# Optimization experiments

Measured on AMD Instinct MI355X. Metric: run time of the kernel, lower is better.

The kernel has to match this reference:

```python
import jax, jax.numpy as jnp
import numpy as np
import math

B, T, D, H, L = 64, 255, 512, 8, 8
CODEBOOK = 512
V = CODEBOOK + 3  # bos/eos/pad
COND_DIM = 512
MAX_LEN = 256
HD = D // H


def _layernorm(x, g, b, eps=1e-5):
    mu = jnp.mean(x, axis=-1, keepdims=True)
    var = jnp.mean(jnp.square(x - mu), axis=-1, keepdims=True)
    return (x - mu) * jax.lax.rsqrt(var + eps) * g + b


def setup_inputs() -> dict:
    key = jax.random.key(0)
    ks = jax.random.split(key, 24)
    s = 0.02
    d = {
        'tokens': jax.random.randint(ks[0], (B, T), 0, V),
        'cond': jax.random.normal(ks[1], (B, COND_DIM), jnp.float32),
        'emb': jax.random.normal(ks[2], (V, D), jnp.float32) * s,  # tied token_emb / head weight
        'pos_emb': jax.random.normal(ks[3], (1, MAX_LEN, D), jnp.float32) * s,
        'cond_w1': jax.random.normal(ks[4], (COND_DIM, D), jnp.float32) * s,
        'cond_b1': jnp.zeros((D,), jnp.float32),
        'cond_w2': jax.random.normal(ks[5], (D, D), jnp.float32) * s,
        'cond_b2': jnp.zeros((D,), jnp.float32),
        'ln1_g': jnp.ones((L, D), jnp.float32),
        'ln1_b': jnp.zeros((L, D), jnp.float32),
        'qkv_w': jax.random.normal(ks[6], (L, D, 3 * D), jnp.float32) * s,
        'qkv_b': jnp.zeros((L, 3 * D), jnp.float32),
        'proj_w': jax.random.normal(ks[7], (L, D, D), jnp.float32) * s,
        'proj_b': jnp.zeros((L, D), jnp.float32),
        'ln2_g': jnp.ones((L, D), jnp.float32),
        'ln2_b': jnp.zeros((L, D), jnp.float32),
        'mlp_w1': jax.random.normal(ks[8], (L, D, 4 * D), jnp.float32) * s,
        'mlp_b1': jnp.zeros((L, 4 * D), jnp.float32),
        'mlp_w2': jax.random.normal(ks[9], (L, 4 * D, D), jnp.float32) * s,
        'mlp_b2': jnp.zeros((L, D), jnp.float32),
        'lnf_g': jnp.ones((D,), jnp.float32),
        'lnf_b': jnp.zeros((D,), jnp.float32),
    }
    return d


def reference(tokens, cond, emb, pos_emb, cond_w1, cond_b1, cond_w2, cond_b2,
              ln1_g, ln1_b, qkv_w, qkv_b, proj_w, proj_b,
              ln2_g, ln2_b, mlp_w1, mlp_b1, mlp_w2, mlp_b2, lnf_g, lnf_b):
    b, t = tokens.shape
    h = emb[tokens] + pos_emb[:, :t, :]                              # [B,T,D]
    c = jax.nn.silu(cond @ cond_w1 + cond_b1) @ cond_w2 + cond_b2    # [B,D]
    h = jnp.concatenate([c[:, None, :], h], axis=1)                  # [B,S,D]
    S = t + 1
    causal = jnp.tril(jnp.ones((S, S), bool))
    scale = 1.0 / math.sqrt(HD)
    for i in range(L):
        x = _layernorm(h, ln1_g[i], ln1_b[i])
        qkv = (x @ qkv_w[i] + qkv_b[i]).reshape(b, S, 3, H, HD).transpose(2, 0, 3, 1, 4)
        q, k, v = qkv[0], qkv[1], qkv[2]                             # [B,H,S,hd]
        a = jnp.einsum('bhsd,bhtd->bhst', q, k) * scale
        a = jnp.where(causal, a, -jnp.inf)
        a = jax.nn.softmax(a, axis=-1)
        o = jnp.einsum('bhst,bhtd->bhsd', a, v).transpose(0, 2, 1, 3).reshape(b, S, D)
        h = h + o @ proj_w[i] + proj_b[i]
        x = _layernorm(h, ln2_g[i], ln2_b[i])
        h = h + jax.nn.gelu(x @ mlp_w1[i] + mlp_b1[i], approximate=False) @ mlp_w2[i] + mlp_b2[i]
    h = _layernorm(h, lnf_g, lnf_b)
    return (h @ emb.T)[:, 1:, :]                                     # [B,T,V]
```

## Files before the change

### kernel.cpp

```cpp
#include <hip/hip_runtime.h>
#include <hip/hip_bf16.h>

typedef __attribute__((ext_vector_type(8))) short bf16x8;
typedef __attribute__((ext_vector_type(4))) float f32x4;
typedef __attribute__((ext_vector_type(4))) unsigned short u16x4;
typedef __attribute__((ext_vector_type(8))) unsigned short u16x8;
typedef unsigned short u16;

#define DEV static __device__ __forceinline__

DEV float bf2f(u16 u) {
  union { unsigned int i; float f; } c; c.i = ((unsigned int)u) << 16; return c.f;
}
DEV u16 f2bf(float f) {
  union { float f; unsigned int i; } c; c.f = f;
  unsigned int i = c.i;
  i += 0x7FFFu + ((i >> 16) & 1u);
  return (u16)(i >> 16);
}

DEV void gload_lds16(const void* g, void* l) {
  __builtin_amdgcn_global_load_lds((const __attribute__((address_space(1))) void*)g,
                                   (__attribute__((address_space(3))) void*)l, 16, 0, 0);
}

DEV f32x4 mfma16(bf16x8 a, bf16x8 b, f32x4 c) {
  return __builtin_amdgcn_mfma_f32_16x16x32_bf16(a, b, c, 0, 0, 0);
}

__global__ __launch_bounds__(256) void ktranspose(const float* __restrict__ in, u16* __restrict__ out,
                                                  int K, int N) {
  __shared__ u16 tile[32][33];
  const float* src = in + (size_t)blockIdx.z * K * N;
  u16* dst = out + (size_t)blockIdx.z * K * N;
  const int n0 = blockIdx.x * 32, k0 = blockIdx.y * 32;
  const int tx = threadIdx.x, ty = threadIdx.y;
#pragma unroll
  for (int i = ty; i < 32; i += 8) tile[i][tx] = f2bf(src[(size_t)(k0 + i) * N + n0 + tx]);
  __syncthreads();
#pragma unroll
  for (int i = ty; i < 32; i += 8) dst[(size_t)(n0 + i) * K + k0 + tx] = tile[tx][i];
}

__global__ __launch_bounds__(256) void kcvt(const float* __restrict__ in, u16* __restrict__ out, int n) {
  int i = blockIdx.x * 256 + threadIdx.x;
  if (i < n) out[i] = f2bf(in[i]);
}

__global__ __launch_bounds__(256) void kcond(const float* __restrict__ cond, const float* __restrict__ w1,
                                             const float* __restrict__ b1, const float* __restrict__ w2,
                                             const float* __restrict__ b2, float* __restrict__ h) {
  __shared__ float xr[512];
  __shared__ float t1[512];
  const int b = blockIdx.x, tid = threadIdx.x;
  for (int i = tid; i < 512; i += 256) xr[i] = cond[b * 512 + i];
  __syncthreads();
  for (int j = tid; j < 512; j += 256) {
    float acc = b1[j];
    for (int k = 0; k < 512; ++k) acc += xr[k] * w1[k * 512 + j];
    t1[j] = acc / (1.f + __expf(-acc));
  }
  __syncthreads();
  for (int j = tid; j < 512; j += 256) {
    float acc = b2[j];
    for (int k = 0; k < 512; ++k) acc += t1[k] * w2[k * 512 + j];
    h[(size_t)b * 256 * 512 + j] = acc;
  }
}

__global__ __launch_bounds__(256) void kembed(const int* __restrict__ tok, const float* __restrict__ emb,
                                              const float* __restrict__ pos, float* __restrict__ h) {
  const int idx = blockIdx.x;
  const int b = idx / 255, t = idx % 255;
  const int c = threadIdx.x * 2;
  const int tk = tok[idx];
  float2 ev = *(const float2*)(emb + (size_t)tk * 512 + c);
  float2 pv = *(const float2*)(pos + (size_t)t * 512 + c);
  float2 r;
  r.x = ev.x + pv.x;
  r.y = ev.y + pv.y;
  *(float2*)(h + ((size_t)b * 256 + 1 + t) * 512 + c) = r;
}

__global__ __launch_bounds__(64) void kln(const float* __restrict__ hin, const float* __restrict__ g,
                                          const float* __restrict__ bt, u16* __restrict__ out) {
  const int row = blockIdx.x, lane = threadIdx.x;
  const float4* x = (const float4*)(hin + (size_t)row * 512);
  float4 v0 = x[lane], v1 = x[lane + 64];
  float s1 = v0.x + v0.y + v0.z + v0.w + v1.x + v1.y + v1.z + v1.w;
  float s2 = v0.x * v0.x + v0.y * v0.y + v0.z * v0.z + v0.w * v0.w +
             v1.x * v1.x + v1.y * v1.y + v1.z * v1.z + v1.w * v1.w;
#pragma unroll
  for (int off = 1; off < 64; off <<= 1) { s1 += __shfl_xor(s1, off); s2 += __shfl_xor(s2, off); }
  float mu = s1 * (1.f / 512.f);
  float var = s2 * (1.f / 512.f) - mu * mu;
  float rs = rsqrtf(var + 1e-5f);
  const int c0 = lane * 4;
  float4 g0 = *(const float4*)(g + c0), g1 = *(const float4*)(g + 256 + c0);
  float4 b0 = *(const float4*)(bt + c0), b1 = *(const float4*)(bt + 256 + c0);
  u16x4 o0, o1;
  o0[0] = f2bf((v0.x - mu) * rs * g0.x + b0.x);
  o0[1] = f2bf((v0.y - mu) * rs * g0.y + b0.y);
  o0[2] = f2bf((v0.z - mu) * rs * g0.z + b0.z);
  o0[3] = f2bf((v0.w - mu) * rs * g0.w + b0.w);
  o1[0] = f2bf((v1.x - mu) * rs * g1.x + b1.x);
  o1[1] = f2bf((v1.y - mu) * rs * g1.y + b1.y);
  o1[2] = f2bf((v1.z - mu) * rs * g1.z + b1.z);
  o1[3] = f2bf((v1.w - mu) * rs * g1.w + b1.w);
  *(u16x4*)(out + (size_t)row * 512 + c0) = o0;
  *(u16x4*)(out + (size_t)row * 512 + 256 + c0) = o1;
}

template<int MODE>
__global__ __launch_bounds__(256, 2) void kgemm(const u16* __restrict__ A, const u16* __restrict__ Bt,
                                                const float* __restrict__ bias, void* __restrict__ Cout,
                                                int M, int N, int K) {
  __shared__ __align__(16) u16 As[2][4096];
  __shared__ __align__(16) u16 Bs[2][4096];
  const int tid = threadIdx.x;
  const int lane = tid & 63;
  const int wr = tid >> 7, wc = (tid >> 6) & 1;
  const int m0 = blockIdx.x * 128, n0 = blockIdx.y * 128;
  const int nkt = K >> 5;
  const int Kb = K * 2;

  const int c0 = tid * 16;
  const int ar0 = c0 >> 6, ao0 = c0 & 63;
  const int ar1 = (c0 + 4096) >> 6, ao1 = (c0 + 4096) & 63;
  int br0 = n0 + ar0, br1 = n0 + ar1;
  if (MODE == 3) { br0 = min(br0, N - 1); br1 = min(br1, N - 1); }
  const char* Ab = (const char*)A;
  const char* Bb = (const char*)Bt;
  const size_t a0 = (size_t)(m0 + ar0) * Kb + ao0;
  const size_t a1 = (size_t)(m0 + ar1) * Kb + ao1;
  const size_t b0 = (size_t)br0 * Kb + ao0;
  const size_t b1 = (size_t)br1 * Kb + ao1;

  f32x4 acc[4][4];
#pragma unroll
  for (int i = 0; i < 4; ++i)
#pragma unroll
    for (int j = 0; j < 4; ++j) acc[i][j] = f32x4{0.f, 0.f, 0.f, 0.f};

  gload_lds16(Ab + a0, (char*)As[0] + c0);
  gload_lds16(Ab + a1, (char*)As[0] + c0 + 4096);
  gload_lds16(Bb + b0, (char*)Bs[0] + c0);
  gload_lds16(Bb + b1, (char*)Bs[0] + c0 + 4096);
  __syncthreads();

  const int aoff = (wr * 64 + (lane & 15)) * 32 + (lane >> 4) * 8;
  const int boff = (wc * 64 + (lane & 15)) * 32 + (lane >> 4) * 8;

  int buf = 0;
  for (int kt = 0; kt < nkt; ++kt) {
    if (kt + 1 < nkt) {
      const size_t ko = (size_t)(kt + 1) * 64;
      gload_lds16(Ab + a0 + ko, (char*)As[buf ^ 1] + c0);
      gload_lds16(Ab + a1 + ko, (char*)As[buf ^ 1] + c0 + 4096);
      gload_lds16(Bb + b0 + ko, (char*)Bs[buf ^ 1] + c0);
      gload_lds16(Bb + b1 + ko, (char*)Bs[buf ^ 1] + c0 + 4096);
    }
    bf16x8 aF[4], bF[4];
#pragma unroll
    for (int mt = 0; mt < 4; ++mt) aF[mt] = *(const bf16x8*)&As[buf][aoff + mt * 512];
#pragma unroll
    for (int nt = 0; nt < 4; ++nt) bF[nt] = *(const bf16x8*)&Bs[buf][boff + nt * 512];
#pragma unroll
    for (int mt = 0; mt < 4; ++mt)
#pragma unroll
      for (int nt = 0; nt < 4; ++nt)
        acc[mt][nt] = mfma16(aF[mt], bF[nt], acc[mt][nt]);
    __syncthreads();
    buf ^= 1;
  }

  float bv[4];
#pragma unroll
  for (int nt = 0; nt < 4; ++nt) {
    int col = n0 + wc * 64 + nt * 16 + (lane & 15);
    bv[nt] = (MODE == 3) ? 0.f : bias[col];
  }

  if (MODE == 0 || MODE == 1) {
    u16* C = (u16*)Cout;
#pragma unroll
    for (int mt = 0; mt < 4; ++mt)
#pragma unroll
      for (int r = 0; r < 4; ++r) {
        int row = m0 + wr * 64 + mt * 16 + (lane >> 4) * 4 + r;
        u16* cp = C + (size_t)row * N + n0 + wc * 64 + (lane & 15);
#pragma unroll
        for (int nt = 0; nt < 4; ++nt) {
          float v = acc[mt][nt][r] + bv[nt];
          if (MODE == 1) v = 0.5f * v * (1.f + erff(v * 0.70710678118f));
          cp[nt * 16] = f2bf(v);
        }
      }
  } else if (MODE == 2) {
    float* hC = (float*)Cout;
#pragma unroll
    for (int mt = 0; mt < 4; ++mt)
#pragma unroll
      for (int r = 0; r < 4; ++r) {
        int row = m0 + wr * 64 + mt * 16 + (lane >> 4) * 4 + r;
        float* hp = hC + (size_t)row * N + n0 + wc * 64 + (lane & 15);
#pragma unroll
        for (int nt = 0; nt < 4; ++nt) hp[nt * 16] += acc[mt][nt][r] + bv[nt];
      }
  } else {
    float* C = (float*)Cout;
#pragma unroll
    for (int mt = 0; mt < 4; ++mt)
#pragma unroll
      for (int r = 0; r < 4; ++r) {
        int row = m0 + wr * 64 + mt * 16 + (lane >> 4) * 4 + r;
        int s = row & 255;
        if (s == 0) continue;
        int bb = row >> 8;
        float* cp = C + ((size_t)bb * 255 + (s - 1)) * 515 + n0 + wc * 64 + (lane & 15);
#pragma unroll
        for (int nt = 0; nt < 4; ++nt) {
          int col = n0 + wc * 64 + nt * 16 + (lane & 15);
          if (col < 515) cp[nt * 16] = acc[mt][nt][r];
        }
      }
  }
}

__global__ __launch_bounds__(256, 1) void kattn(const u16* __restrict__ qkv, u16* __restrict__ o) {
  __shared__ __align__(16) u16 Ks[256][72];
  __shared__ __align__(16) u16 Vt[64][264];
  __shared__ __align__(16) u16 Ps[4][64][72];
  const int tid = threadIdx.x, wv = tid >> 6, lane = tid & 63;
  const int bh = blockIdx.x, bb = bh >> 3, hh = bh & 7;
  const size_t base = (size_t)bb * 256 * 1536 + hh * 64;

  for (int c = tid; c < 2048; c += 256) {
    int s = c >> 3, pp = c & 7;
    u16x8 kv = *(const u16x8*)(qkv + base + (size_t)s * 1536 + 512 + pp * 8);
    *(u16x8*)&Ks[s][pp * 8] = kv;
    u16x8 vv = *(const u16x8*)(qkv + base + (size_t)s * 1536 + 1024 + pp * 8);
#pragma unroll
    for (int j = 0; j < 8; ++j) Vt[pp * 8 + j][s] = vv[j];
  }
  __syncthreads();

  bf16x8 qf[4][2];
#pragma unroll
  for (int mt = 0; mt < 4; ++mt)
#pragma unroll
    for (int ks = 0; ks < 2; ++ks)
      qf[mt][ks] = *(const bf16x8*)(qkv + base +
                   (size_t)(wv * 64 + mt * 16 + (lane & 15)) * 1536 + ks * 32 + (lane >> 4) * 8);

  const float scale = 0.125f;
  float mrow[4][4], lsum[4][4];
#pragma unroll
  for (int mt = 0; mt < 4; ++mt)
#pragma unroll
    for (int r = 0; r < 4; ++r) { mrow[mt][r] = -1e30f; lsum[mt][r] = 0.f; }

  for (int ct = 0; ct <= wv; ++ct) {
    f32x4 sacc[4][4];
#pragma unroll
    for (int i = 0; i < 4; ++i)
#pragma unroll
      for (int j = 0; j < 4; ++j) sacc[i][j] = f32x4{0.f, 0.f, 0.f, 0.f};
#pragma unroll
    for (int ks = 0; ks < 2; ++ks) {
      bf16x8 kf[4];
#pragma unroll
      for (int nt = 0; nt < 4; ++nt)
        kf[nt] = *(const bf16x8*)&Ks[ct * 64 + nt * 16 + (lane & 15)][ks * 32 + (lane >> 4) * 8];
#pragma unroll
      for (int mt = 0; mt < 4; ++mt)
#pragma unroll
        for (int nt = 0; nt < 4; ++nt)
          sacc[mt][nt] = mfma16(qf[mt][ks], kf[nt], sacc[mt][nt]);
    }
#pragma unroll
    for (int mt = 0; mt < 4; ++mt)
#pragma unroll
      for (int r = 0; r < 4; ++r) {
        int srow = wv * 64 + mt * 16 + (lane >> 4) * 4 + r;
        float mx = -1e30f;
#pragma unroll
        for (int nt = 0; nt < 4; ++nt) {
          int tcol = ct * 64 + nt * 16 + (lane & 15);
          float v = sacc[mt][nt][r] * scale;
          if (tcol > srow) v = -1e30f;
          mx = fmaxf(mx, v);
        }
#pragma unroll
        for (int off = 1; off < 16; off <<= 1) mx = fmaxf(mx, __shfl_xor(mx, off));
        mrow[mt][r] = fmaxf(mrow[mt][r], mx);
      }
  }

  f32x4 oacc[4][4];
#pragma unroll
  for (int i = 0; i < 4; ++i)
#pragma unroll
    for (int j = 0; j < 4; ++j) oacc[i][j] = f32x4{0.f, 0.f, 0.f, 0.f};

  for (int ct = 0; ct <= wv; ++ct) {
    f32x4 sacc[4][4];
#pragma unroll
    for (int i = 0; i < 4; ++i)
#pragma unroll
      for (int j = 0; j < 4; ++j) sacc[i][j] = f32x4{0.f, 0.f, 0.f, 0.f};
#pragma unroll
    for (int ks = 0; ks < 2; ++ks) {
      bf16x8 kf[4];
#pragma unroll
      for (int nt = 0; nt < 4; ++nt)
        kf[nt] = *(const bf16x8*)&Ks[ct * 64 + nt * 16 + (lane & 15)][ks * 32 + (lane >> 4) * 8];
#pragma unroll
      for (int mt = 0; mt < 4; ++mt)
#pragma unroll
        for (int nt = 0; nt < 4; ++nt)
          sacc[mt][nt] = mfma16(qf[mt][ks], kf[nt], sacc[mt][nt]);
    }
#pragma unroll
    for (int mt = 0; mt < 4; ++mt)
#pragma unroll
      for (int r = 0; r < 4; ++r) {
        int srow = wv * 64 + mt * 16 + (lane >> 4) * 4 + r;
        float ps = 0.f;
#pragma unroll
        for (int nt = 0; nt < 4; ++nt) {
          int tcol = ct * 64 + nt * 16 + (lane & 15);
          float v = sacc[mt][nt][r] * scale;
          float pe = (tcol > srow) ? 0.f : __expf(v - mrow[mt][r]);
          ps += pe;
          Ps[wv][mt * 16 + (lane >> 4) * 4 + r][nt * 16 + (lane & 15)] = f2bf(pe);
        }
#pragma unroll
        for (int off = 1; off < 16; off <<= 1) ps += __shfl_xor(ps, off);
        lsum[mt][r] += ps;
      }
#pragma unroll
    for (int ks = 0; ks < 2; ++ks) {
      bf16x8 pf[4], vf[4];
#pragma unroll
      for (int mt = 0; mt < 4; ++mt)
        pf[mt] = *(const bf16x8*)&Ps[wv][mt * 16 + (lane & 15)][ks * 32 + (lane >> 4) * 8];
#pragma unroll
      for (int nt = 0; nt < 4; ++nt)
        vf[nt] = *(const bf16x8*)&Vt[nt * 16 + (lane & 15)][ct * 64 + ks * 32 + (lane >> 4) * 8];
#pragma unroll
      for (int mt = 0; mt < 4; ++mt)
#pragma unroll
        for (int nt = 0; nt < 4; ++nt)
          oacc[mt][nt] = mfma16(pf[mt], vf[nt], oacc[mt][nt]);
    }
  }

#pragma unroll
  for (int mt = 0; mt < 4; ++mt)
#pragma unroll
    for (int r = 0; r < 4; ++r) {
      int s = wv * 64 + mt * 16 + (lane >> 4) * 4 + r;
      float inv = 1.f / lsum[mt][r];
      u16* op = o + ((size_t)bb * 256 + s) * 512 + hh * 64 + (lane & 15);
#pragma unroll
      for (int nt = 0; nt < 4; ++nt) op[nt * 16] = f2bf(oacc[mt][nt][r] * inv);
    }
}

extern "C" void kernel_launch(void* const* d_in, const int* in_sizes, int n_in,
                              void* d_out, int out_size, void* d_ws, size_t ws_size,
                              hipStream_t stream) {
  const int* tokens = (const int*)d_in[0];
  const float* cond = (const float*)d_in[1];
  const float* emb = (const float*)d_in[2];
  const float* pos = (const float*)d_in[3];
  const float* cw1 = (const float*)d_in[4];
  const float* cb1 = (const float*)d_in[5];
  const float* cw2 = (const float*)d_in[6];
  const float* cb2 = (const float*)d_in[7];
  const float* ln1g = (const float*)d_in[8];
  const float* ln1b = (const float*)d_in[9];
  const float* qkvw = (const float*)d_in[10];
  const float* qkvb = (const float*)d_in[11];
  const float* projw = (const float*)d_in[12];
  const float* projb = (const float*)d_in[13];
  const float* ln2g = (const float*)d_in[14];
  const float* ln2b = (const float*)d_in[15];
  const float* w1 = (const float*)d_in[16];
  const float* b1 = (const float*)d_in[17];
  const float* w2 = (const float*)d_in[18];
  const float* b2 = (const float*)d_in[19];
  const float* lnfg = (const float*)d_in[20];
  const float* lnfb = (const float*)d_in[21];

  const size_t NEEDED = (size_t)16384 * 512 * 4
                      + (size_t)16384 * 512 * 2
                      + (size_t)16384 * 2048 * 2
                      + (size_t)8 * 1536 * 512 * 2
                      + (size_t)8 * 512 * 512 * 2
                      + (size_t)8 * 2048 * 512 * 2
                      + (size_t)8 * 512 * 2048 * 2;
  if (ws_size < NEEDED) return;

  char* p = (char*)d_ws;
  float* h = (float*)p;        p += (size_t)16384 * 512 * 4;
  u16* xln = (u16*)p;          p += (size_t)16384 * 512 * 2;
  u16* big = (u16*)p;          p += (size_t)16384 * 2048 * 2;
  u16* attn_o = big + (size_t)16384 * 1536;
  u16* embB = big;
  u16* qkvT = (u16*)p;         p += (size_t)8 * 1536 * 512 * 2;
  u16* projT = (u16*)p;        p += (size_t)8 * 512 * 512 * 2;
  u16* w1T = (u16*)p;          p += (size_t)8 * 2048 * 512 * 2;
  u16* w2T = (u16*)p;          p += (size_t)8 * 512 * 2048 * 2;

  ktranspose<<<dim3(48, 16, 8), dim3(32, 8), 0, stream>>>(qkvw, qkvT, 512, 1536);
  ktranspose<<<dim3(16, 16, 8), dim3(32, 8), 0, stream>>>(projw, projT, 512, 512);
  ktranspose<<<dim3(64, 16, 8), dim3(32, 8), 0, stream>>>(w1, w1T, 512, 2048);
  ktranspose<<<dim3(16, 64, 8), dim3(32, 8), 0, stream>>>(w2, w2T, 2048, 512);

  kembed<<<16320, 256, 0, stream>>>(tokens, emb, pos, h);
  kcond<<<64, 256, 0, stream>>>(cond, cw1, cb1, cw2, cb2, h);

  for (int l = 0; l < 8; ++l) {
    kln<<<16384, 64, 0, stream>>>(h, ln1g + l * 512, ln1b + l * 512, xln);
    kgemm<0><<<dim3(128, 12), 256, 0, stream>>>(xln, qkvT + (size_t)l * 1536 * 512,
                                                qkvb + l * 1536, big, 16384, 1536, 512);
    kattn<<<512, 256, 0, stream>>>(big, attn_o);
    kgemm<2><<<dim3(128, 4), 256, 0, stream>>>(attn_o, projT + (size_t)l * 512 * 512,
                                               projb + l * 512, h, 16384, 512, 512);
    kln<<<16384, 64, 0, stream>>>(h, ln2g + l * 512, ln2b + l * 512, xln);
    kgemm<1><<<dim3(128, 16), 256, 0, stream>>>(xln, w1T + (size_t)l * 2048 * 512,
                                                b1 + l * 2048, big, 16384, 2048, 512);
    kgemm<2><<<dim3(128, 4), 256, 0, stream>>>(big, w2T + (size_t)l * 512 * 2048,
                                               b2 + l * 512, h, 16384, 512, 2048);
  }
  kln<<<16384, 64, 0, stream>>>(h, lnfg, lnfb, xln);
  kcvt<<<1030, 256, 0, stream>>>(emb, embB, 515 * 512);
  kgemm<3><<<dim3(128, 5), 256, 0, stream>>>(xln, embB, nullptr, d_out, 16384, 515, 512);
}
```

Baseline: 2.018 ms.

## Triple-buffer GEMM with swizzled LDS, batch layernorm rows, fast erf GELU

```diff
diff --git a/kernel.cpp b/kernel.cpp
--- a/kernel.cpp
+++ b/kernel.cpp
@@ -27,6 +27,16 @@
 DEV f32x4 mfma16(bf16x8 a, bf16x8 b, f32x4 c) {
   return __builtin_amdgcn_mfma_f32_16x16x32_bf16(a, b, c, 0, 0, 0);
 }
+
+DEV float fasterf(float x) {
+  float ax = fabsf(x);
+  float t = 1.0f / (1.0f + 0.3275911f * ax);
+  float y = t * (0.254829592f + t * (-0.284496736f + t * (1.421413741f +
+            t * (-1.453152027f + t * 1.061405429f))));
+  float r = 1.0f - y * __expf(-ax * ax);
+  return copysignf(r, x);
+}
+DEV float gelu(float v) { return 0.5f * v * (1.0f + fasterf(v * 0.70710678118f)); }
 
 __global__ __launch_bounds__(256) void ktranspose(const float* __restrict__ in, u16* __restrict__ out,
                                                   int K, int N) {
@@ -82,9 +92,9 @@
   *(float2*)(h + ((size_t)b * 256 + 1 + t) * 512 + c) = r;
 }
 
-__global__ __launch_bounds__(64) void kln(const float* __restrict__ hin, const float* __restrict__ g,
-                                          const float* __restrict__ bt, u16* __restrict__ out) {
-  const int row = blockIdx.x, lane = threadIdx.x;
+__global__ __launch_bounds__(256) void kln(const float* __restrict__ hin, const float* __restrict__ g,
+                                           const float* __restrict__ bt, u16* __restrict__ out) {
+  const int row = blockIdx.x * 4 + (threadIdx.x >> 6), lane = threadIdx.x & 63;
   const float4* x = (const float4*)(hin + (size_t)row * 512);
   float4 v0 = x[lane], v1 = x[lane + 64];
   float s1 = v0.x + v0.y + v0.z + v0.w + v1.x + v1.y + v1.z + v1.w;
@@ -112,29 +122,30 @@
 }
 
 template<int MODE>
-__global__ __launch_bounds__(256, 2) void kgemm(const u16* __restrict__ A, const u16* __restrict__ Bt,
-                                                const float* __restrict__ bias, void* __restrict__ Cout,
-                                                int M, int N, int K) {
-  __shared__ __align__(16) u16 As[2][4096];
-  __shared__ __align__(16) u16 Bs[2][4096];
+__global__ __launch_bounds__(256, 2) void kgemm3(const u16* __restrict__ A, const u16* __restrict__ Bt,
+                                                 const float* __restrict__ bias, void* __restrict__ Cout,
+                                                 int M, int N, int K) {
+  __shared__ __align__(16) u16 As[3][4096];
+  __shared__ __align__(16) u16 Bs[3][4096];
   const int tid = threadIdx.x;
   const int lane = tid & 63;
   const int wr = tid >> 7, wc = (tid >> 6) & 1;
   const int m0 = blockIdx.x * 128, n0 = blockIdx.y * 128;
   const int nkt = K >> 5;
-  const int Kb = K * 2;
-
-  const int c0 = tid * 16;
-  const int ar0 = c0 >> 6, ao0 = c0 & 63;
-  const int ar1 = (c0 + 4096) >> 6, ao1 = (c0 + 4096) & 63;
-  int br0 = n0 + ar0, br1 = n0 + ar1;
-  if (MODE == 3) { br0 = min(br0, N - 1); br1 = min(br1, N - 1); }
+  const size_t Kb = (size_t)K * 2;
+
+  const int srow = tid >> 2;
+  const int schunk = tid & 3;
+  const int sc = schunk ^ ((srow >> 1) & 3);
+  const int d1 = tid * 16, d2 = tid * 16 + 4096;
+  int brA = n0 + srow, brB = n0 + srow + 64;
+  if (MODE == 3) { brA = min(brA, N - 1); brB = min(brB, N - 1); }
   const char* Ab = (const char*)A;
   const char* Bb = (const char*)Bt;
-  const size_t a0 = (size_t)(m0 + ar0) * Kb + ao0;
-  const size_t a1 = (size_t)(m0 + ar1) * Kb + ao1;
-  const size_t b0 = (size_t)br0 * Kb + ao0;
-  const size_t b1 = (size_t)br1 * Kb + ao1;
+  const size_t a0 = (size_t)(m0 + srow) * Kb + sc * 16;
+  const size_t a1 = (size_t)(m0 + srow + 64) * Kb + sc * 16;
+  const size_t b0 = (size_t)brA * Kb + sc * 16;
+  const size_t b1 = (size_t)brB * Kb + sc * 16;
 
   f32x4 acc[4][4];
 #pragma unroll
@@ -142,36 +153,52 @@
 #pragma unroll
     for (int j = 0; j < 4; ++j) acc[i][j] = f32x4{0.f, 0.f, 0.f, 0.f};
 
-  gload_lds16(Ab + a0, (char*)As[0] + c0);
-  gload_lds16(Ab + a1, (char*)As[0] + c0 + 4096);
-  gload_lds16(Bb + b0, (char*)Bs[0] + c0);
-  gload_lds16(Bb + b1, (char*)Bs[0] + c0 + 4096);
-  __syncthreads();
-
-  const int aoff = (wr * 64 + (lane & 15)) * 32 + (lane >> 4) * 8;
-  const int boff = (wc * 64 + (lane & 15)) * 32 + (lane >> 4) * 8;
-
-  int buf = 0;
+#pragma unroll
+  for (int t = 0; t < 2; ++t) {
+    const size_t ko = (size_t)t * 64;
+    gload_lds16(Ab + a0 + ko, (char*)As[t] + d1);
+    gload_lds16(Ab + a1 + ko, (char*)As[t] + d2);
+    gload_lds16(Bb + b0 + ko, (char*)Bs[t] + d1);
+    gload_lds16(Bb + b1 + ko, (char*)Bs[t] + d2);
+  }
+  asm volatile("s_waitcnt vmcnt(4)" ::: "memory");
+  __builtin_amdgcn_s_barrier();
+  __builtin_amdgcn_sched_barrier(0);
+
+  const int kchunk = (((lane >> 4) ^ ((lane >> 1) & 3)) << 4);
+  const int arow = wr * 64 + (lane & 15);
+  const int brow = wc * 64 + (lane & 15);
+
   for (int kt = 0; kt < nkt; ++kt) {
-    if (kt + 1 < nkt) {
-      const size_t ko = (size_t)(kt + 1) * 64;
-      gload_lds16(Ab + a0 + ko, (char*)As[buf ^ 1] + c0);
-      gload_lds16(Ab + a1 + ko, (char*)As[buf ^ 1] + c0 + 4096);
-      gload_lds16(Bb + b0 + ko, (char*)Bs[buf ^ 1] + c0);
-      gload_lds16(Bb + b1 + ko, (char*)Bs[buf ^ 1] + c0 + 4096);
-    }
+    const int bufc = kt % 3;
+    const bool deep = (kt + 2 < nkt);
+    if (deep) {
+      const int bufn = (kt + 2) % 3;
+      const size_t ko = (size_t)(kt + 2) * 64;
+      gload_lds16(Ab + a0 + ko, (char*)As[bufn] + d1);
+      gload_lds16(Ab + a1 + ko, (char*)As[bufn] + d2);
+      gload_lds16(Bb + b0 + ko, (char*)Bs[bufn] + d1);
+      gload_lds16(Bb + b1 + ko, (char*)Bs[bufn] + d2);
+    }
+    const char* Ap = (const char*)As[bufc];
+    const char* Bp = (const char*)Bs[bufc];
     bf16x8 aF[4], bF[4];
 #pragma unroll
-    for (int mt = 0; mt < 4; ++mt) aF[mt] = *(const bf16x8*)&As[buf][aoff + mt * 512];
-#pragma unroll
-    for (int nt = 0; nt < 4; ++nt) bF[nt] = *(const bf16x8*)&Bs[buf][boff + nt * 512];
+    for (int mt = 0; mt < 4; ++mt) aF[mt] = *(const bf16x8*)(Ap + (arow + mt * 16) * 64 + kchunk);
+#pragma unroll
+    for (int nt = 0; nt < 4; ++nt) bF[nt] = *(const bf16x8*)(Bp + (brow + nt * 16) * 64 + kchunk);
 #pragma unroll
     for (int mt = 0; mt < 4; ++mt)
 #pragma unroll
       for (int nt = 0; nt < 4; ++nt)
         acc[mt][nt] = mfma16(aF[mt], bF[nt], acc[mt][nt]);
-    __syncthreads();
-    buf ^= 1;
+    if (deep) {
+      asm volatile("s_waitcnt vmcnt(4)" ::: "memory");
+    } else {
+      asm volatile("s_waitcnt vmcnt(0)" ::: "memory");
+    }
+    __builtin_amdgcn_s_barrier();
+    __builtin_amdgcn_sched_barrier(0);
   }
 
   float bv[4];
@@ -192,7 +219,7 @@
 #pragma unroll
         for (int nt = 0; nt < 4; ++nt) {
           float v = acc[mt][nt][r] + bv[nt];
-          if (MODE == 1) v = 0.5f * v * (1.f + erff(v * 0.70710678118f));
+          if (MODE == 1) v = gelu(v);
           cp[nt * 16] = f2bf(v);
         }
       }
@@ -423,19 +450,19 @@
   kcond<<<64, 256, 0, stream>>>(cond, cw1, cb1, cw2, cb2, h);
 
   for (int l = 0; l < 8; ++l) {
-    kln<<<16384, 64, 0, stream>>>(h, ln1g + l * 512, ln1b + l * 512, xln);
-    kgemm<0><<<dim3(128, 12), 256, 0, stream>>>(xln, qkvT + (size_t)l * 1536 * 512,
-                                                qkvb + l * 1536, big, 16384, 1536, 512);
+    kln<<<4096, 256, 0, stream>>>(h, ln1g + l * 512, ln1b + l * 512, xln);
+    kgemm3<0><<<dim3(128, 12), 256, 0, stream>>>(xln, qkvT + (size_t)l * 1536 * 512,
+                                                 qkvb + l * 1536, big, 16384, 1536, 512);
     kattn<<<512, 256, 0, stream>>>(big, attn_o);
-    kgemm<2><<<dim3(128, 4), 256, 0, stream>>>(attn_o, projT + (size_t)l * 512 * 512,
-                                               projb + l * 512, h, 16384, 512, 512);
-    kln<<<16384, 64, 0, stream>>>(h, ln2g + l * 512, ln2b + l * 512, xln);
-    kgemm<1><<<dim3(128, 16), 256, 0, stream>>>(xln, w1T + (size_t)l * 2048 * 512,
-                                                b1 + l * 2048, big, 16384, 2048, 512);
-    kgemm<2><<<dim3(128, 4), 256, 0, stream>>>(big, w2T + (size_t)l * 512 * 2048,
-                                               b2 + l * 512, h, 16384, 512, 2048);
-  }
-  kln<<<16384, 64, 0, stream>>>(h, lnfg, lnfb, xln);
+    kgemm3<2><<<dim3(128, 4), 256, 0, stream>>>(attn_o, projT + (size_t)l * 512 * 512,
+                                                projb + l * 512, h, 16384, 512, 512);
+    kln<<<4096, 256, 0, stream>>>(h, ln2g + l * 512, ln2b + l * 512, xln);
+    kgemm3<1><<<dim3(128, 16), 256, 0, stream>>>(xln, w1T + (size_t)l * 2048 * 512,
+                                                 b1 + l * 2048, big, 16384, 2048, 512);
+    kgemm3<2><<<dim3(128, 4), 256, 0, stream>>>(big, w2T + (size_t)l * 512 * 2048,
+                                                b2 + l * 512, h, 16384, 512, 2048);
+  }
+  kln<<<4096, 256, 0, stream>>>(h, lnfg, lnfb, xln);
   kcvt<<<1030, 256, 0, stream>>>(emb, embB, 515 * 512);
-  kgemm<3><<<dim3(128, 5), 256, 0, stream>>>(xln, embB, nullptr, d_out, 16384, 515, 512);
-}
+  kgemm3<3><<<dim3(128, 5), 256, 0, stream>>>(xln, embB, nullptr, d_out, 16384, 515, 512);
+}
```

Result: slower. 2.104 ms (+4.2%).
